# Performance work log

Hardware: AMD Instinct MI355X
Metric: run time of the kernel (lower is better)

The kernel has to match this reference:

```python
import jax, jax.numpy as jnp
import numpy as np

N_NODES = 100000
N_EDGES = 1600000
D_IN = 128
D_OUT = 128


def setup_inputs() -> dict:
    key = jax.random.key(0)
    ks = jax.random.split(key, 6)
    x = jax.random.normal(ks[0], (N_NODES, D_IN), dtype=jnp.float32)
    edge_row = jax.random.randint(ks[1], (N_EDGES,), 0, N_NODES, dtype=jnp.int32)
    edge_col = jax.random.randint(ks[2], (N_EDGES,), 0, N_NODES, dtype=jnp.int32)
    # normalized adjacency values (e.g. 1/deg), roughly uniform small positives
    edge_val = jax.random.uniform(ks[3], (N_EDGES,), dtype=jnp.float32) * (1.0 / 16.0)
    # torch Linear weight is [out,in]; we store transposed [in,out] for x @ W
    scale = float(np.sqrt(6.0 / (D_IN + D_OUT)))  # xavier_uniform
    W_local = jax.random.uniform(ks[4], (D_IN, D_OUT), dtype=jnp.float32, minval=-scale, maxval=scale)
    W_neigh = jax.random.uniform(ks[5], (D_IN, D_OUT), dtype=jnp.float32, minval=-scale, maxval=scale)
    b_local = jnp.zeros((D_OUT,), dtype=jnp.float32)
    b_neigh = jnp.zeros((D_OUT,), dtype=jnp.float32)
    return {"x": x, "edge_row": edge_row, "edge_col": edge_col, "edge_val": edge_val,
            "W_local": W_local, "b_local": b_local, "W_neigh": W_neigh, "b_neigh": b_neigh}


def reference(x, edge_row, edge_col, edge_val, W_local, b_local, W_neigh, b_neigh):
    # feat_trans_local = linear_local(x)
    local = x @ W_local + b_local  # [N, D_OUT]
    # sparse.mm(edge_norm, x): out[r] += val * x[c]  (COO SpMM via gather + segment_sum)
    msgs = edge_val[:, None] * x[edge_col]  # [E, D_IN]
    agg = jax.ops.segment_sum(msgs, edge_row, num_segments=N_NODES)  # [N, D_IN]
    neigh = agg @ W_neigh + b_neigh  # [N, D_OUT]
    out = jnp.concatenate([local, neigh], axis=1)  # [N, 2*D_OUT]
    return jax.nn.relu(out)
```

## Files before the change

kernel.cpp:

```cpp
#include <hip/hip_runtime.h>
#include <hip/hip_bf16.h>

#define D 128
#define WPAD 136
#define RPC 64
#define RPC_SHIFT 6
#define CAPC 1280
#define NCMAX 2048
#define P1_BLOCKS 256

typedef __attribute__((ext_vector_type(8))) short short8;
typedef __attribute__((ext_vector_type(8))) __bf16 bf16x8;
typedef __attribute__((ext_vector_type(4))) float float4_t;

__device__ __forceinline__ short f2bf(float f) {
    __hip_bfloat16 b = __float2bfloat16(f);
    return __builtin_bit_cast(short, b);
}

__device__ __forceinline__ short8 load_frag8(const float* p) {
    const float4_t* q = reinterpret_cast<const float4_t*>(p);
    float4_t u = q[0], v = q[1];
    short8 r;
    r[0] = f2bf(u[0]); r[1] = f2bf(u[1]); r[2] = f2bf(u[2]); r[3] = f2bf(u[3]);
    r[4] = f2bf(v[0]); r[5] = f2bf(v[1]); r[6] = f2bf(v[2]); r[7] = f2bf(v[3]);
    return r;
}

__device__ __forceinline__ float4_t mfma_bf16(short8 a, short8 b, float4_t c) {
    return __builtin_amdgcn_mfma_f32_16x16x32_bf16(
        __builtin_bit_cast(bf16x8, a), __builtin_bit_cast(bf16x8, b), c, 0, 0, 0);
}

__device__ __forceinline__ float bf_lo(unsigned u) { return __uint_as_float(u << 16); }
__device__ __forceinline__ float bf_hi(unsigned u) { return __uint_as_float(u & 0xFFFF0000u); }

__global__ __launch_bounds__(256) void gemm_kernel(
    const float* __restrict__ x,
    const float* __restrict__ Wl, const float* __restrict__ bl,
    const float* __restrict__ Wn,
    float* __restrict__ out, unsigned short* __restrict__ y,
    int* __restrict__ gcur, int ncoarse, int N)
{
    __shared__ short lW[D * WPAD];

    int gid = blockIdx.x * 256 + threadIdx.x;
    if (gid < ncoarse) gcur[gid] = 0;

    for (int i = threadIdx.x; i < D * D; i += 256) {
        int k = i >> 7, n = i & (D - 1);
        lW[n * WPAD + k] = f2bf(Wl[i]);
    }

    int wave = threadIdx.x >> 6;
    int lane = threadIdx.x & 63;
    int quad = lane >> 4;
    int l16  = lane & 15;
    int rbase = blockIdx.x * 128 + wave * 32;

    short8 ax[2][4];
    for (int m = 0; m < 2; ++m) {
        int row  = rbase + m * 16 + l16;
        int rowc = row < N ? row : N - 1;
        const float* xp = x + (size_t)rowc * D + quad * 8;
        for (int t = 0; t < 4; ++t) ax[m][t] = load_frag8(xp + t * 32);
    }
    __syncthreads();

    for (int nt = 0; nt < 8; ++nt) {
        int colc = nt * 16 + l16;
        float4_t acc[2];
        acc[0] = acc[1] = (float4_t){0.f, 0.f, 0.f, 0.f};
        const short* bp = lW + colc * WPAD + quad * 8;
        for (int t = 0; t < 4; ++t) {
            short8 bf = *reinterpret_cast<const short8*>(bp + t * 32);
            acc[0] = mfma_bf16(ax[0][t], bf, acc[0]);
            acc[1] = mfma_bf16(ax[1][t], bf, acc[1]);
        }
        float bLc = bl[colc];
        for (int m = 0; m < 2; ++m) {
            int row0 = rbase + m * 16 + quad * 4;
            for (int i = 0; i < 4; ++i) {
                int rr = row0 + i;
                if (rr < N) {
                    float lv = acc[m][i] + bLc;
                    out[(size_t)rr * 256 + colc] = lv > 0.f ? lv : 0.f;
                }
            }
        }
    }
    __syncthreads();

    for (int i = threadIdx.x; i < D * D; i += 256) {
        int k = i >> 7, n = i & (D - 1);
        lW[n * WPAD + k] = f2bf(Wn[i]);
    }
    __syncthreads();

    for (int nt = 0; nt < 8; ++nt) {
        int colc = nt * 16 + l16;
        float4_t acc[2];
        acc[0] = acc[1] = (float4_t){0.f, 0.f, 0.f, 0.f};
        const short* bp = lW + colc * WPAD + quad * 8;
        for (int t = 0; t < 4; ++t) {
            short8 bf = *reinterpret_cast<const short8*>(bp + t * 32);
            acc[0] = mfma_bf16(ax[0][t], bf, acc[0]);
            acc[1] = mfma_bf16(ax[1][t], bf, acc[1]);
        }
        for (int m = 0; m < 2; ++m) {
            int row0 = rbase + m * 16 + quad * 4;
            for (int i = 0; i < 4; ++i) {
                int rr = row0 + i;
                if (rr < N)
                    y[(size_t)rr * D + colc] = (unsigned short)f2bf(acc[m][i]);
            }
        }
    }
}

__global__ __launch_bounds__(256) void coarse_scatter(
    const int* __restrict__ erow, const int* __restrict__ ecol,
    const float* __restrict__ eval, int* __restrict__ gcur,
    int2* __restrict__ pairs1, int E, int ncoarse)
{
    __shared__ int hist[NCMAX];
    __shared__ int base[NCMAX];
    int tid = threadIdx.x;
    for (int i = tid; i < ncoarse; i += 256) hist[i] = 0;
    __syncthreads();

    int chunk = (E + P1_BLOCKS - 1) / P1_BLOCKS;
    int e0 = blockIdx.x * chunk;
    int e1 = e0 + chunk; e1 = e1 < E ? e1 : E;

    for (int e = e0 + tid; e < e1; e += 256)
        atomicAdd(&hist[erow[e] >> RPC_SHIFT], 1);
    __syncthreads();

    for (int i = tid; i < ncoarse; i += 256) {
        int h = hist[i];
        base[i] = h ? atomicAdd(&gcur[i], h) : 0;
        hist[i] = 0;
    }
    __syncthreads();

    for (int e = e0 + tid; e < e1; e += 256) {
        int r = erow[e];
        int c = r >> RPC_SHIFT;
        int pos = atomicAdd(&hist[c], 1) + base[c];
        if (pos < CAPC) {
            int key = ((r & (RPC - 1)) << 17) | ecol[e];
            pairs1[(size_t)c * CAPC + pos] = make_int2(key, __float_as_int(eval[e]));
        }
    }
}

__global__ __launch_bounds__(256) void bucket_gather(
    const unsigned short* __restrict__ y, const int* __restrict__ gcur,
    const int2* __restrict__ pairs1, const float* __restrict__ bn,
    float* __restrict__ out, int N)
{
    __shared__ unsigned short bidx[CAPC];
    __shared__ int hist[RPC];
    __shared__ int off[RPC];
    __shared__ int cur[RPC];

    int tid  = threadIdx.x;
    int wave = tid >> 6;
    int lane = tid & 63;
    int c    = blockIdx.x;

    if (tid < RPC) { hist[tid] = 0; cur[tid] = 0; }
    __syncthreads();

    int cnt = gcur[c];
    cnt = cnt < CAPC ? cnt : CAPC;
    const int2* pb = pairs1 + (size_t)c * CAPC;

    for (int j = tid; j < cnt; j += 256)
        atomicAdd(&hist[(pb[j].x >> 17) & (RPC - 1)], 1);
    __syncthreads();

    if (tid == 0) {
        int run = 0;
        for (int g = 0; g < RPC; ++g) { off[g] = run; run += hist[g]; }
    }
    __syncthreads();

    for (int j = tid; j < cnt; j += 256) {
        int g = (pb[j].x >> 17) & (RPC - 1);
        int pos = atomicAdd(&cur[g], 1) + off[g];
        bidx[pos] = (unsigned short)j;
    }
    __syncthreads();

    const unsigned* yv = reinterpret_cast<const unsigned*>(y);
    float2 bnv = reinterpret_cast<const float2*>(bn)[lane];

    for (int rr = 0; rr < RPC / 4; ++rr) {
        int g  = wave * (RPC / 4) + rr;
        int j0 = off[g];
        int n  = hist[g];
        float a0x = 0.f, a0y = 0.f, a1x = 0.f, a1y = 0.f;
        int j = 0;
        for (; j + 3 < n; j += 4) {
            int2 p0 = pb[bidx[j0 + j    ]];
            int2 p1 = pb[bidx[j0 + j + 1]];
            int2 p2 = pb[bidx[j0 + j + 2]];
            int2 p3 = pb[bidx[j0 + j + 3]];
            unsigned t0 = yv[(size_t)(p0.x & 0x1FFFF) * 64 + lane];
            unsigned t1 = yv[(size_t)(p1.x & 0x1FFFF) * 64 + lane];
            unsigned t2 = yv[(size_t)(p2.x & 0x1FFFF) * 64 + lane];
            unsigned t3 = yv[(size_t)(p3.x & 0x1FFFF) * 64 + lane];
            float v0 = __int_as_float(p0.y), v1 = __int_as_float(p1.y);
            float v2 = __int_as_float(p2.y), v3 = __int_as_float(p3.y);
            a0x += v0 * bf_lo(t0); a0y += v0 * bf_hi(t0);
            a1x += v1 * bf_lo(t1); a1y += v1 * bf_hi(t1);
            a0x += v2 * bf_lo(t2); a0y += v2 * bf_hi(t2);
            a1x += v3 * bf_lo(t3); a1y += v3 * bf_hi(t3);
        }
        for (; j < n; ++j) {
            int2 p = pb[bidx[j0 + j]];
            unsigned t = yv[(size_t)(p.x & 0x1FFFF) * 64 + lane];
            float v = __int_as_float(p.y);
            a0x += v * bf_lo(t); a0y += v * bf_hi(t);
        }
        int node = c * RPC + g;
        if (node < N) {
            float s0 = a0x + a1x + bnv.x;
            float s1 = a0y + a1y + bnv.y;
            float2 ov;
            ov.x = s0 > 0.f ? s0 : 0.f;
            ov.y = s1 > 0.f ? s1 : 0.f;
            reinterpret_cast<float2*>(out + (size_t)node * 256 + D)[lane] = ov;
        }
    }
}

extern "C" void kernel_launch(void* const* d_in, const int* in_sizes, int n_in,
                              void* d_out, int out_size, void* d_ws, size_t ws_size,
                              hipStream_t stream) {
    const float* x    = (const float*)d_in[0];
    const int*   erow = (const int*)  d_in[1];
    const int*   ecol = (const int*)  d_in[2];
    const float* eval = (const float*)d_in[3];
    const float* Wl   = (const float*)d_in[4];
    const float* bl   = (const float*)d_in[5];
    const float* Wn   = (const float*)d_in[6];
    const float* bn   = (const float*)d_in[7];
    float*       out  = (float*)d_out;

    int N = in_sizes[0] / D;
    int E = in_sizes[1];
    int ncoarse = (N + RPC - 1) >> RPC_SHIFT;

    char* ws = (char*)d_ws;
    size_t off_y   = 0;
    size_t off_p1  = off_y  + (size_t)N * D * sizeof(short);
    size_t off_gc  = off_p1 + (size_t)ncoarse * CAPC * sizeof(int2);

    unsigned short* y = (unsigned short*)(ws + off_y);
    int2* pairs1 = (int2*)(ws + off_p1);
    int*  gcur   = (int*)(ws + off_gc);

    int gblocks = (N + 127) / 128;
    gemm_kernel<<<gblocks, 256, 0, stream>>>(x, Wl, bl, Wn, out, y, gcur, ncoarse, N);

    coarse_scatter<<<P1_BLOCKS, 256, 0, stream>>>(erow, ecol, eval, gcur, pairs1, E, ncoarse);

    bucket_gather<<<ncoarse, 256, 0, stream>>>(y, gcur, pairs1, bn, out, N);
}
```

Before: 330.3 us.

## Fuse GEMM and edge scatter into one launch, split gather buckets, vectorize stores

Merges the coarse edge-bucketing scatter into the GEMM kernel as extra leading blocks, so the two independent phases run concurrently in a single launch, and moves the counter reset to a memset. The MFMA operands are swapped so each lane holds four consecutive output columns, which allows float4 and 4xbf16 vector stores instead of scalar strided ones. The gather kernel now uses two blocks per 64-row bucket for more parallelism and unrolls 8 edge loads to raise memory-level parallelism. The cost is that each gather block re-reads the whole bucket's pairs, plus an extra memset launch.

```diff
diff --git a/kernel.cpp b/kernel.cpp
--- a/kernel.cpp
+++ b/kernel.cpp
@@ -10,6 +10,7 @@
 #define P1_BLOCKS 256
 
 typedef __attribute__((ext_vector_type(8))) short short8;
+typedef __attribute__((ext_vector_type(4))) short sh4;
 typedef __attribute__((ext_vector_type(8))) __bf16 bf16x8;
 typedef __attribute__((ext_vector_type(4))) float float4_t;
 
@@ -35,17 +36,54 @@
 __device__ __forceinline__ float bf_lo(unsigned u) { return __uint_as_float(u << 16); }
 __device__ __forceinline__ float bf_hi(unsigned u) { return __uint_as_float(u & 0xFFFF0000u); }
 
-__global__ __launch_bounds__(256) void gemm_kernel(
+__global__ __launch_bounds__(256) void fused_gemm_scatter(
     const float* __restrict__ x,
     const float* __restrict__ Wl, const float* __restrict__ bl,
     const float* __restrict__ Wn,
+    const int* __restrict__ erow, const int* __restrict__ ecol,
+    const float* __restrict__ eval,
     float* __restrict__ out, unsigned short* __restrict__ y,
-    int* __restrict__ gcur, int ncoarse, int N)
+    int* __restrict__ gcur, int2* __restrict__ pairs1,
+    int E, int ncoarse, int N)
 {
-    __shared__ short lW[D * WPAD];
-
-    int gid = blockIdx.x * 256 + threadIdx.x;
-    if (gid < ncoarse) gcur[gid] = 0;
+    __shared__ int smem[D * WPAD / 2];
+
+    if (blockIdx.x < P1_BLOCKS) {
+        int* hist = smem;
+        int* base = smem + NCMAX;
+        int tid = threadIdx.x;
+        for (int i = tid; i < ncoarse; i += 256) hist[i] = 0;
+        __syncthreads();
+
+        int chunk = (E + P1_BLOCKS - 1) / P1_BLOCKS;
+        int e0 = blockIdx.x * chunk;
+        int e1 = e0 + chunk; e1 = e1 < E ? e1 : E;
+
+        for (int e = e0 + tid; e < e1; e += 256)
+            atomicAdd(&hist[erow[e] >> RPC_SHIFT], 1);
+        __syncthreads();
+
+        for (int i = tid; i < ncoarse; i += 256) {
+            int h = hist[i];
+            base[i] = h ? atomicAdd(&gcur[i], h) : 0;
+            hist[i] = 0;
+        }
+        __syncthreads();
+
+        for (int e = e0 + tid; e < e1; e += 256) {
+            int r = erow[e];
+            int c = r >> RPC_SHIFT;
+            int pos = atomicAdd(&hist[c], 1) + base[c];
+            if (pos < CAPC) {
+                int key = ((r & (RPC - 1)) << 17) | ecol[e];
+                pairs1[(size_t)c * CAPC + pos] = make_int2(key, __float_as_int(eval[e]));
+            }
+        }
+        return;
+    }
+
+    short* lW = reinterpret_cast<short*>(smem);
+    int gb = blockIdx.x - P1_BLOCKS;
 
     for (int i = threadIdx.x; i < D * D; i += 256) {
         int k = i >> 7, n = i & (D - 1);
@@ -56,7 +94,7 @@
     int lane = threadIdx.x & 63;
     int quad = lane >> 4;
     int l16  = lane & 15;
-    int rbase = blockIdx.x * 128 + wave * 32;
+    int rbase = gb * 128 + wave * 32;
 
     short8 ax[2][4];
     for (int m = 0; m < 2; ++m) {
@@ -69,23 +107,27 @@
 
     for (int nt = 0; nt < 8; ++nt) {
         int colc = nt * 16 + l16;
-        float4_t acc[2];
-        acc[0] = acc[1] = (float4_t){0.f, 0.f, 0.f, 0.f};
+        float4_t acc0 = {0.f, 0.f, 0.f, 0.f};
+        float4_t acc1 = {0.f, 0.f, 0.f, 0.f};
         const short* bp = lW + colc * WPAD + quad * 8;
         for (int t = 0; t < 4; ++t) {
             short8 bf = *reinterpret_cast<const short8*>(bp + t * 32);
-            acc[0] = mfma_bf16(ax[0][t], bf, acc[0]);
-            acc[1] = mfma_bf16(ax[1][t], bf, acc[1]);
-        }
-        float bLc = bl[colc];
+            acc0 = mfma_bf16(bf, ax[0][t], acc0);
+            acc1 = mfma_bf16(bf, ax[1][t], acc1);
+        }
+        float4_t blv = *reinterpret_cast<const float4_t*>(bl + nt * 16 + quad * 4);
+        int col0 = nt * 16 + quad * 4;
         for (int m = 0; m < 2; ++m) {
-            int row0 = rbase + m * 16 + quad * 4;
-            for (int i = 0; i < 4; ++i) {
-                int rr = row0 + i;
-                if (rr < N) {
-                    float lv = acc[m][i] + bLc;
-                    out[(size_t)rr * 256 + colc] = lv > 0.f ? lv : 0.f;
+            int row = rbase + m * 16 + l16;
+            if (row < N) {
+                float4_t a = m ? acc1 : acc0;
+                float4_t ov;
+                #pragma unroll
+                for (int i = 0; i < 4; ++i) {
+                    float lv = a[i] + blv[i];
+                    ov[i] = lv > 0.f ? lv : 0.f;
                 }
+                *reinterpret_cast<float4_t*>(out + (size_t)row * 256 + col0) = ov;
             }
         }
     }
@@ -99,58 +141,24 @@
 
     for (int nt = 0; nt < 8; ++nt) {
         int colc = nt * 16 + l16;
-        float4_t acc[2];
-        acc[0] = acc[1] = (float4_t){0.f, 0.f, 0.f, 0.f};
+        float4_t acc0 = {0.f, 0.f, 0.f, 0.f};
+        float4_t acc1 = {0.f, 0.f, 0.f, 0.f};
         const short* bp = lW + colc * WPAD + quad * 8;
         for (int t = 0; t < 4; ++t) {
             short8 bf = *reinterpret_cast<const short8*>(bp + t * 32);
-            acc[0] = mfma_bf16(ax[0][t], bf, acc[0]);
-            acc[1] = mfma_bf16(ax[1][t], bf, acc[1]);
-        }
+            acc0 = mfma_bf16(bf, ax[0][t], acc0);
+            acc1 = mfma_bf16(bf, ax[1][t], acc1);
+        }
+        int col0 = nt * 16 + quad * 4;
         for (int m = 0; m < 2; ++m) {
-            int row0 = rbase + m * 16 + quad * 4;
-            for (int i = 0; i < 4; ++i) {
-                int rr = row0 + i;
-                if (rr < N)
-                    y[(size_t)rr * D + colc] = (unsigned short)f2bf(acc[m][i]);
-            }
-        }
-    }
-}
-
-__global__ __launch_bounds__(256) void coarse_scatter(
-    const int* __restrict__ erow, const int* __restrict__ ecol,
-    const float* __restrict__ eval, int* __restrict__ gcur,
-    int2* __restrict__ pairs1, int E, int ncoarse)
-{
-    __shared__ int hist[NCMAX];
-    __shared__ int base[NCMAX];
-    int tid = threadIdx.x;
-    for (int i = tid; i < ncoarse; i += 256) hist[i] = 0;
-    __syncthreads();
-
-    int chunk = (E + P1_BLOCKS - 1) / P1_BLOCKS;
-    int e0 = blockIdx.x * chunk;
-    int e1 = e0 + chunk; e1 = e1 < E ? e1 : E;
-
-    for (int e = e0 + tid; e < e1; e += 256)
-        atomicAdd(&hist[erow[e] >> RPC_SHIFT], 1);
-    __syncthreads();
-
-    for (int i = tid; i < ncoarse; i += 256) {
-        int h = hist[i];
-        base[i] = h ? atomicAdd(&gcur[i], h) : 0;
-        hist[i] = 0;
-    }
-    __syncthreads();
-
-    for (int e = e0 + tid; e < e1; e += 256) {
-        int r = erow[e];
-        int c = r >> RPC_SHIFT;
-        int pos = atomicAdd(&hist[c], 1) + base[c];
-        if (pos < CAPC) {
-            int key = ((r & (RPC - 1)) << 17) | ecol[e];
-            pairs1[(size_t)c * CAPC + pos] = make_int2(key, __float_as_int(eval[e]));
+            int row = rbase + m * 16 + l16;
+            if (row < N) {
+                float4_t a = m ? acc1 : acc0;
+                sh4 s;
+                #pragma unroll
+                for (int i = 0; i < 4; ++i) s[i] = f2bf(a[i]);
+                *reinterpret_cast<sh4*>(y + (size_t)row * 128 + col0) = s;
+            }
         }
     }
 }
@@ -161,63 +169,68 @@
     float* __restrict__ out, int N)
 {
     __shared__ unsigned short bidx[CAPC];
-    __shared__ int hist[RPC];
-    __shared__ int off[RPC];
-    __shared__ int cur[RPC];
+    __shared__ int hist[32];
+    __shared__ int off[32];
+    __shared__ int cur[32];
 
     int tid  = threadIdx.x;
     int wave = tid >> 6;
     int lane = tid & 63;
-    int c    = blockIdx.x;
-
-    if (tid < RPC) { hist[tid] = 0; cur[tid] = 0; }
+    int b    = blockIdx.x;
+    int c    = b >> 1;
+    int half = b & 1;
+
+    if (tid < 32) { hist[tid] = 0; cur[tid] = 0; }
     __syncthreads();
 
     int cnt = gcur[c];
     cnt = cnt < CAPC ? cnt : CAPC;
     const int2* pb = pairs1 + (size_t)c * CAPC;
 
-    for (int j = tid; j < cnt; j += 256)
-        atomicAdd(&hist[(pb[j].x >> 17) & (RPC - 1)], 1);
+    for (int j = tid; j < cnt; j += 256) {
+        int g = (pb[j].x >> 17) & (RPC - 1);
+        if ((g >> 5) == half) atomicAdd(&hist[g & 31], 1);
+    }
     __syncthreads();
 
     if (tid == 0) {
         int run = 0;
-        for (int g = 0; g < RPC; ++g) { off[g] = run; run += hist[g]; }
+        for (int g = 0; g < 32; ++g) { off[g] = run; run += hist[g]; }
     }
     __syncthreads();
 
     for (int j = tid; j < cnt; j += 256) {
         int g = (pb[j].x >> 17) & (RPC - 1);
-        int pos = atomicAdd(&cur[g], 1) + off[g];
-        bidx[pos] = (unsigned short)j;
+        if ((g >> 5) == half) {
+            int pos = atomicAdd(&cur[g & 31], 1) + off[g & 31];
+            bidx[pos] = (unsigned short)j;
+        }
     }
     __syncthreads();
 
     const unsigned* yv = reinterpret_cast<const unsigned*>(y);
     float2 bnv = reinterpret_cast<const float2*>(bn)[lane];
 
-    for (int rr = 0; rr < RPC / 4; ++rr) {
-        int g  = wave * (RPC / 4) + rr;
-        int j0 = off[g];
-        int n  = hist[g];
+    for (int rr = 0; rr < 8; ++rr) {
+        int gl = wave * 8 + rr;
+        int j0 = off[gl];
+        int n  = hist[gl];
         float a0x = 0.f, a0y = 0.f, a1x = 0.f, a1y = 0.f;
         int j = 0;
-        for (; j + 3 < n; j += 4) {
-            int2 p0 = pb[bidx[j0 + j    ]];
-            int2 p1 = pb[bidx[j0 + j + 1]];
-            int2 p2 = pb[bidx[j0 + j + 2]];
-            int2 p3 = pb[bidx[j0 + j + 3]];
-            unsigned t0 = yv[(size_t)(p0.x & 0x1FFFF) * 64 + lane];
-            unsigned t1 = yv[(size_t)(p1.x & 0x1FFFF) * 64 + lane];
-            unsigned t2 = yv[(size_t)(p2.x & 0x1FFFF) * 64 + lane];
-            unsigned t3 = yv[(size_t)(p3.x & 0x1FFFF) * 64 + lane];
-            float v0 = __int_as_float(p0.y), v1 = __int_as_float(p1.y);
-            float v2 = __int_as_float(p2.y), v3 = __int_as_float(p3.y);
-            a0x += v0 * bf_lo(t0); a0y += v0 * bf_hi(t0);
-            a1x += v1 * bf_lo(t1); a1y += v1 * bf_hi(t1);
-            a0x += v2 * bf_lo(t2); a0y += v2 * bf_hi(t2);
-            a1x += v3 * bf_lo(t3); a1y += v3 * bf_hi(t3);
+        for (; j + 7 < n; j += 8) {
+            int2 p[8];
+            unsigned t[8];
+            #pragma unroll
+            for (int u = 0; u < 8; ++u) p[u] = pb[bidx[j0 + j + u]];
+            #pragma unroll
+            for (int u = 0; u < 8; ++u)
+                t[u] = yv[(size_t)(p[u].x & 0x1FFFF) * 64 + lane];
+            #pragma unroll
+            for (int u = 0; u < 8; ++u) {
+                float v = __int_as_float(p[u].y);
+                if (u & 1) { a1x += v * bf_lo(t[u]); a1y += v * bf_hi(t[u]); }
+                else       { a0x += v * bf_lo(t[u]); a0y += v * bf_hi(t[u]); }
+            }
         }
         for (; j < n; ++j) {
             int2 p = pb[bidx[j0 + j]];
@@ -225,7 +238,7 @@
             float v = __int_as_float(p.y);
             a0x += v * bf_lo(t); a0y += v * bf_hi(t);
         }
-        int node = c * RPC + g;
+        int node = c * RPC + half * 32 + gl;
         if (node < N) {
             float s0 = a0x + a1x + bnv.x;
             float s1 = a0y + a1y + bnv.y;
@@ -263,10 +276,11 @@
     int2* pairs1 = (int2*)(ws + off_p1);
     int*  gcur   = (int*)(ws + off_gc);
 
+    hipMemsetAsync(gcur, 0, (size_t)ncoarse * sizeof(int), stream);
+
     int gblocks = (N + 127) / 128;
-    gemm_kernel<<<gblocks, 256, 0, stream>>>(x, Wl, bl, Wn, out, y, gcur, ncoarse, N);
-
-    coarse_scatter<<<P1_BLOCKS, 256, 0, stream>>>(erow, ecol, eval, gcur, pairs1, E, ncoarse);
-
-    bucket_gather<<<ncoarse, 256, 0, stream>>>(y, gcur, pairs1, bn, out, N);
-}
+    fused_gemm_scatter<<<P1_BLOCKS + gblocks, 256, 0, stream>>>(
+        x, Wl, bl, Wn, erow, ecol, eval, out, y, gcur, pairs1, E, ncoarse, N);
+
+    bucket_gather<<<ncoarse * 2, 256, 0, stream>>>(y, gcur, pairs1, bn, out, N);
+}
```

Result: no change. 324.5 us (-1.8%).
